# Optimization experiments

Measured on AMD Instinct MI355X. Metric: run time of the kernel, lower is better.

## Reference

```python
import jax, jax.numpy as jnp
import numpy as np

M, N, C, D = 2, 8, 1024, 256  # n_routers, num_adapters, channel_dim, down_sample_size
B, S = 32, 512


def setup_inputs() -> dict:
    key = jax.random.key(0)
    k1, k2, k3, k4, k5 = jax.random.split(key, 5)
    x = jax.random.normal(k1, (B, S, C), dtype=jnp.float32)
    expert_index = jax.random.randint(k2, (M, B), 0, N, dtype=jnp.int32)
    down_w = jax.random.normal(k3, (M, N, C, D), dtype=jnp.float32) * 0.01
    down_b = jax.random.normal(k4, (M, N, D), dtype=jnp.float32) * 0.01
    up_w = jax.random.normal(k5, (M, N, D, C), dtype=jnp.float32) * 0.01
    return {"x": x, "expert_index": expert_index, "down_w": down_w,
            "down_b": down_b, "up_w": up_w}


def reference(x, expert_index, down_w, down_b, up_w):
    # Gather per-(router, batch-element) adapter weights along the adapter axis.
    idx = expert_index  # [M, B]
    bw_down = jnp.take_along_axis(down_w, idx[:, :, None, None], axis=1)  # [M, B, C, D]
    bb_down = jnp.take_along_axis(down_b, idx[:, :, None], axis=1)        # [M, B, D]
    bw_up = jnp.take_along_axis(up_w, idx[:, :, None, None], axis=1)      # [M, B, D, C]
    # z = swish(x @ W_down + b_down)  -> [M, B, S, D]
    z = jnp.einsum('bsc,mbcd->mbsd', x, bw_down) + bb_down[:, :, None, :]
    z = jax.nn.silu(z)
    # u = z @ W_up -> [M, B, S, C]
    u = jnp.einsum('mbsd,mbdc->mbsc', z, bw_up)
    return u
```

## Files before the change

### kernel.cpp

```cpp
#include <hip/hip_runtime.h>
#include <stdint.h>

typedef unsigned short u16;
typedef __bf16 bf16x8 __attribute__((ext_vector_type(8)));
typedef float f32x4 __attribute__((ext_vector_type(4)));

#define MM 2
#define NN 8
#define CC 1024
#define DD 256
#define BB 32
#define SS 512

__device__ __forceinline__ u16 f2bf(float f) {
  uint32_t u = __float_as_uint(f);
  u += 0x7FFFu + ((u >> 16) & 1u);
  return (u16)(u >> 16);
}

__device__ __forceinline__ uint32_t pack2(float a, float b) {
  return (uint32_t)f2bf(a) | ((uint32_t)f2bf(b) << 16);
}

__device__ __forceinline__ void async16(const void* g, void* l) {
  __builtin_amdgcn_global_load_lds(
      (const __attribute__((address_space(1))) uint32_t*)g,
      (__attribute__((address_space(3))) uint32_t*)l, 16, 0, 0);
}

#define T_BLOCKS 4096
__global__ __launch_bounds__(256) void prep_w(
    const float* __restrict__ dw, u16* __restrict__ wdT,
    const float* __restrict__ uw, u16* __restrict__ wuT) {
  const int bid = blockIdx.x;
  __shared__ float tile[32][33];
  const float* src;
  u16* dst;
  int R, L, bx, by, slab;
  if (bid < T_BLOCKS) {
    int t = bid;
    slab = t >> 8;
    int t2 = t & 255;
    bx = t2 & 7;  by = t2 >> 3;
    R = CC; L = DD;
    src = dw; dst = wdT;
  } else {
    int t = bid - T_BLOCKS;
    slab = t >> 8;
    int t2 = t & 255;
    bx = t2 & 31; by = t2 >> 5;
    R = DD; L = CC;
    src = uw; dst = wuT;
  }
  src += (size_t)slab * R * L;
  dst += (size_t)slab * R * L;
  const int c0 = bx * 32, r0 = by * 32;
  const int tx = threadIdx.x & 31, ty = threadIdx.x >> 5;
#pragma unroll
  for (int i = 0; i < 32; i += 8)
    tile[ty + i][tx] = src[(size_t)(r0 + ty + i) * L + c0 + tx];
  __syncthreads();
#pragma unroll
  for (int i = 0; i < 32; i += 8)
    dst[(size_t)(c0 + ty + i) * R + r0 + tx] = f2bf(tile[tx][ty + i]);
}

__global__ __launch_bounds__(512, 2) void fused_adapter(
    const float* __restrict__ x, const u16* __restrict__ wdT,
    const u16* __restrict__ wuT, const float* __restrict__ db,
    const int* __restrict__ eidx, float* __restrict__ out) {
  __shared__ __align__(16) u16 smA[2][128 * 32];
  __shared__ __align__(16) u16 smB[2][256 * 32];
  __shared__ __align__(16) u16 zl[8 * 128 * 32];

  const int pair = blockIdx.y;
  const int m = pair >> 5;
  const int b = pair & 31;
  const int e = eidx[pair];
  const int s0 = blockIdx.x * 128;

  const int tid = threadIdx.x;
  const int lane = tid & 63;
  const int wave = tid >> 6;
  const int quad = lane >> 4;
  const int l16 = lane & 15;

  const int srow = lane >> 2;
  const int kc = (lane & 3) * 8;

  const int wr = (wave >> 2) * 64;
  const int wc = (wave & 3) * 64;

  const u16* Bd = wdT + (size_t)(m * NN + e) * DD * CC;
  const u16* Bu = wuT + (size_t)(m * NN + e) * CC * DD;

  const int arow = tid >> 2;
  const int akseg = (tid & 3) * 8;
  const float* gAx = x + ((size_t)b * SS + s0 + arow) * CC + akseg;
  const int lAoff = arow * 32 + akseg;

  const u16* gB0 = Bd + (size_t)(wave * 32 + srow) * CC + kc;
  const u16* gB1 = Bd + (size_t)(wave * 32 + 16 + srow) * CC + kc;
  const int lB0o = (wave * 32) * 32;
  const int lB1o = (wave * 32 + 16) * 32;

  f32x4 acc[4][4];
#pragma unroll
  for (int i = 0; i < 4; ++i)
#pragma unroll
    for (int j = 0; j < 4; ++j) acc[i][j] = (f32x4){0.f, 0.f, 0.f, 0.f};

  {
    float4 a0 = *reinterpret_cast<const float4*>(gAx + 0);
    float4 a1 = *reinterpret_cast<const float4*>(gAx + 4);
    *reinterpret_cast<uint4*>(&smA[0][lAoff]) =
        make_uint4(pack2(a0.x, a0.y), pack2(a0.z, a0.w),
                   pack2(a1.x, a1.y), pack2(a1.z, a1.w));
  }
  async16(gB0, &smB[0][lB0o]);
  async16(gB1, &smB[0][lB1o]);
  __syncthreads();

  for (int kk = 0; kk < 32; ++kk) {
    const int cur = kk & 1, nxt = cur ^ 1;
    float4 n0, n1;
    if (kk < 31) {
      const int ko = (kk + 1) * 32;
      n0 = *reinterpret_cast<const float4*>(gAx + ko + 0);
      n1 = *reinterpret_cast<const float4*>(gAx + ko + 4);
      async16(gB0 + ko, &smB[nxt][lB0o]);
      async16(gB1 + ko, &smB[nxt][lB1o]);
    } else {
      async16(Bu + (size_t)(wave * 32 + srow) * DD + kc, &smB[nxt][lB0o]);
      async16(Bu + (size_t)(wave * 32 + 16 + srow) * DD + kc, &smB[nxt][lB1o]);
    }
    bf16x8 af[4], bfr[4];
#pragma unroll
    for (int i = 0; i < 4; ++i)
      af[i] = *reinterpret_cast<const bf16x8*>(&smA[cur][(wr + i * 16 + l16) * 32 + quad * 8]);
#pragma unroll
    for (int j = 0; j < 4; ++j)
      bfr[j] = *reinterpret_cast<const bf16x8*>(&smB[cur][(wc + j * 16 + l16) * 32 + quad * 8]);
#pragma unroll
    for (int i = 0; i < 4; ++i)
#pragma unroll
      for (int j = 0; j < 4; ++j)
        acc[i][j] = __builtin_amdgcn_mfma_f32_16x16x32_bf16(af[i], bfr[j], acc[i][j], 0, 0, 0);
    if (kk < 31) {
      *reinterpret_cast<uint4*>(&smA[nxt][lAoff]) =
          make_uint4(pack2(n0.x, n0.y), pack2(n0.z, n0.w),
                     pack2(n1.x, n1.y), pack2(n1.z, n1.w));
    }
    __syncthreads();
  }

  const float* bias_p = db + (size_t)(m * NN + e) * DD;
#pragma unroll
  for (int j = 0; j < 4; ++j) {
    const int d = wc + j * 16 + l16;
    const float bias = bias_p[d];
    const int kt = d >> 5;
    const int kl = d & 31;
#pragma unroll
    for (int i = 0; i < 4; ++i) {
      const int zr = wr + i * 16 + quad * 4;
#pragma unroll
      for (int r = 0; r < 4; ++r) {
        float v = acc[i][j][r] + bias;
        v = v / (1.f + __expf(-v));
        zl[(kt * 128 + zr + r) * 32 + kl] = f2bf(v);
      }
    }
  }
  __syncthreads();

  float* ob = out + ((size_t)pair * SS + s0) * CC;

  for (int g = 0; g < 32; ++g) {
    const int cur2 = g & 1, nxt2 = cur2 ^ 1;
    const int ct = g >> 3;
    const int it = g & 7;
    if (g < 31) {
      const int g2 = g + 1;
      const int ct2 = g2 >> 3;
      const int ko2 = (g2 & 7) * 32;
      async16(Bu + (size_t)(ct2 * 256 + wave * 32 + srow) * DD + ko2 + kc, &smB[nxt2][lB0o]);
      async16(Bu + (size_t)(ct2 * 256 + wave * 32 + 16 + srow) * DD + ko2 + kc, &smB[nxt2][lB1o]);
    }
    if (it == 0) {
#pragma unroll
      for (int i = 0; i < 4; ++i)
#pragma unroll
        for (int j = 0; j < 4; ++j) acc[i][j] = (f32x4){0.f, 0.f, 0.f, 0.f};
    }
    bf16x8 af[4], bfr[4];
#pragma unroll
    for (int i = 0; i < 4; ++i)
      af[i] = *reinterpret_cast<const bf16x8*>(&zl[(it * 128 + wr + i * 16 + l16) * 32 + quad * 8]);
#pragma unroll
    for (int j = 0; j < 4; ++j)
      bfr[j] = *reinterpret_cast<const bf16x8*>(&smB[cur2][(wc + j * 16 + l16) * 32 + quad * 8]);
#pragma unroll
    for (int i = 0; i < 4; ++i)
#pragma unroll
      for (int j = 0; j < 4; ++j)
        acc[i][j] = __builtin_amdgcn_mfma_f32_16x16x32_bf16(af[i], bfr[j], acc[i][j], 0, 0, 0);
    if (it == 7) {
#pragma unroll
      for (int j = 0; j < 4; ++j) {
        const int c = ct * 256 + wc + j * 16 + l16;
#pragma unroll
        for (int i = 0; i < 4; ++i) {
          const int sr = wr + i * 16 + quad * 4;
#pragma unroll
          for (int r = 0; r < 4; ++r)
            ob[(size_t)(sr + r) * CC + c] = acc[i][j][r];
        }
      }
    }
    __syncthreads();
  }
}

extern "C" void kernel_launch(void* const* d_in, const int* in_sizes, int n_in,
                              void* d_out, int out_size, void* d_ws, size_t ws_size,
                              hipStream_t stream) {
  const float* x  = (const float*)d_in[0];
  const int* eidx = (const int*)d_in[1];
  const float* dw = (const float*)d_in[2];
  const float* db = (const float*)d_in[3];
  const float* uw = (const float*)d_in[4];
  float* out = (float*)d_out;

  char* ws = (char*)d_ws;
  u16* wdT = (u16*)(ws);
  u16* wuT = (u16*)(ws + (size_t)8 * 1024 * 1024);

  prep_w<<<dim3(2 * T_BLOCKS), dim3(256), 0, stream>>>(dw, wdT, uw, wuT);
  fused_adapter<<<dim3(SS / 128, MM * BB), dim3(512), 0, stream>>>(
      x, wdT, wuT, db, eidx, out);
}
```

Baseline: 271.5 us.

## Halve row tile, swizzle LDS layouts, interleave routers, widen prep transpose tiles

The fused adapter kernel now processes 64 sequence rows per block instead of 128. This halves the LDS footprint and accumulators so four blocks can share a CU, and it doubles the grid. LDS tiles for x, weights and the intermediate z use an XOR swizzle on the 8-element k-slots to cut bank conflicts, and the block index is remapped so both routers for the same batch element run adjacently and share x in cache. The weight prep kernel transposes 64x32 tiles and writes packed bf16 pairs as 32-bit stores. Smaller tiles mean each block reloads the full per-expert weights for fewer rows, which raises weight traffic.

Result: slower. 278.7 us (+2.7%).

```diff
diff --git a/kernel.cpp b/kernel.cpp
--- a/kernel.cpp
+++ b/kernel.cpp
@@ -28,94 +28,92 @@
       (__attribute__((address_space(3))) uint32_t*)l, 16, 0, 0);
 }
 
-#define T_BLOCKS 4096
 __global__ __launch_bounds__(256) void prep_w(
     const float* __restrict__ dw, u16* __restrict__ wdT,
     const float* __restrict__ uw, u16* __restrict__ wuT) {
-  const int bid = blockIdx.x;
-  __shared__ float tile[32][33];
-  const float* src;
-  u16* dst;
-  int R, L, bx, by, slab;
-  if (bid < T_BLOCKS) {
-    int t = bid;
-    slab = t >> 8;
-    int t2 = t & 255;
-    bx = t2 & 7;  by = t2 >> 3;
-    R = CC; L = DD;
-    src = dw; dst = wdT;
+  __shared__ float tile[64][33];
+  int bid = blockIdx.x;
+  const float* src; u16* dst; int K, N, tk, tn;
+  if (bid < 2048) {
+    K = CC; N = DD;
+    const int slab = bid >> 7, t = bid & 127;
+    tk = t >> 3; tn = t & 7;
+    src = dw + (size_t)slab * K * N;
+    dst = wdT + (size_t)slab * K * N;
   } else {
-    int t = bid - T_BLOCKS;
-    slab = t >> 8;
-    int t2 = t & 255;
-    bx = t2 & 31; by = t2 >> 5;
-    R = DD; L = CC;
-    src = uw; dst = wuT;
-  }
-  src += (size_t)slab * R * L;
-  dst += (size_t)slab * R * L;
-  const int c0 = bx * 32, r0 = by * 32;
+    bid -= 2048;
+    K = DD; N = CC;
+    const int slab = bid >> 7, t = bid & 127;
+    tk = t >> 5; tn = t & 31;
+    src = uw + (size_t)slab * K * N;
+    dst = wuT + (size_t)slab * K * N;
+  }
+  const int k0 = tk * 64, n0 = tn * 32;
   const int tx = threadIdx.x & 31, ty = threadIdx.x >> 5;
 #pragma unroll
-  for (int i = 0; i < 32; i += 8)
-    tile[ty + i][tx] = src[(size_t)(r0 + ty + i) * L + c0 + tx];
+  for (int i = 0; i < 64; i += 8)
+    tile[ty + i][tx] = src[(size_t)(k0 + ty + i) * N + n0 + tx];
   __syncthreads();
-#pragma unroll
-  for (int i = 0; i < 32; i += 8)
-    dst[(size_t)(c0 + ty + i) * R + r0 + tx] = f2bf(tile[tx][ty + i]);
-}
-
-__global__ __launch_bounds__(512, 2) void fused_adapter(
+  uint32_t* dst32 = reinterpret_cast<uint32_t*>(dst);
+#pragma unroll
+  for (int i = 0; i < 32; i += 8) {
+    const int nr = ty + i;
+    dst32[((size_t)(n0 + nr) * K + k0) / 2 + tx] =
+        pack2(tile[2 * tx][nr], tile[2 * tx + 1][nr]);
+  }
+}
+
+__global__ __launch_bounds__(512, 4) void fused_adapter(
     const float* __restrict__ x, const u16* __restrict__ wdT,
     const u16* __restrict__ wuT, const float* __restrict__ db,
     const int* __restrict__ eidx, float* __restrict__ out) {
-  __shared__ __align__(16) u16 smA[2][128 * 32];
+  __shared__ __align__(16) u16 smA[2][64 * 32];
   __shared__ __align__(16) u16 smB[2][256 * 32];
-  __shared__ __align__(16) u16 zl[8 * 128 * 32];
+  __shared__ __align__(16) u16 zl[8 * 64 * 32];
 
   const int pair = blockIdx.y;
-  const int m = pair >> 5;
-  const int b = pair & 31;
-  const int e = eidx[pair];
-  const int s0 = blockIdx.x * 128;
+  const int m = pair & 1;
+  const int b = pair >> 1;
+  const int mb = m * BB + b;
+  const int e = eidx[mb];
+  const int s0 = blockIdx.x * 64;
 
   const int tid = threadIdx.x;
   const int lane = tid & 63;
   const int wave = tid >> 6;
   const int quad = lane >> 4;
   const int l16 = lane & 15;
-
-  const int srow = lane >> 2;
-  const int kc = (lane & 3) * 8;
-
-  const int wr = (wave >> 2) * 64;
+  const int fx = (l16 >> 1) & 3;
+
+  const int wr = (wave >> 2) * 32;
   const int wc = (wave & 3) * 64;
 
   const u16* Bd = wdT + (size_t)(m * NN + e) * DD * CC;
   const u16* Bu = wuT + (size_t)(m * NN + e) * CC * DD;
 
-  const int arow = tid >> 2;
-  const int akseg = (tid & 3) * 8;
+  const int arow = tid >> 3;
+  const int akseg = (tid & 7) * 4;
   const float* gAx = x + ((size_t)b * SS + s0 + arow) * CC + akseg;
-  const int lAoff = arow * 32 + akseg;
-
-  const u16* gB0 = Bd + (size_t)(wave * 32 + srow) * CC + kc;
-  const u16* gB1 = Bd + (size_t)(wave * 32 + 16 + srow) * CC + kc;
-  const int lB0o = (wave * 32) * 32;
-  const int lB1o = (wave * 32 + 16) * 32;
-
-  f32x4 acc[4][4];
-#pragma unroll
-  for (int i = 0; i < 4; ++i)
+  const int lAoff = arow * 32 +
+                    ((((tid & 7) >> 1) ^ ((arow >> 1) & 3)) * 8) + (tid & 1) * 4;
+
+  const int srow = lane >> 2;
+  const int qx = (lane & 3) ^ ((srow >> 1) & 3);
+  const u16* gB0 = Bd + (size_t)(wave * 32 + srow) * CC + qx * 8;
+  const u16* gB1 = gB0 + (size_t)16 * CC;
+  const int lB0o = wave * 32 * 32;
+  const int lB1o = lB0o + 16 * 32;
+
+  f32x4 acc[2][4];
+#pragma unroll
+  for (int i = 0; i < 2; ++i)
 #pragma unroll
     for (int j = 0; j < 4; ++j) acc[i][j] = (f32x4){0.f, 0.f, 0.f, 0.f};
 
   {
-    float4 a0 = *reinterpret_cast<const float4*>(gAx + 0);
-    float4 a1 = *reinterpret_cast<const float4*>(gAx + 4);
-    *reinterpret_cast<uint4*>(&smA[0][lAoff]) =
-        make_uint4(pack2(a0.x, a0.y), pack2(a0.z, a0.w),
-                   pack2(a1.x, a1.y), pack2(a1.z, a1.w));
+    float4 a0 = *reinterpret_cast<const float4*>(gAx);
+    uint2 w; w.x = pack2(a0.x, a0.y); w.y = pack2(a0.z, a0.w);
+    *reinterpret_cast<uint2*>(&smA[0][lAoff]) = w;
   }
   async16(gB0, &smB[0][lB0o]);
   async16(gB1, &smB[0][lB1o]);
@@ -123,33 +121,33 @@
 
   for (int kk = 0; kk < 32; ++kk) {
     const int cur = kk & 1, nxt = cur ^ 1;
-    float4 n0, n1;
+    float4 nA;
     if (kk < 31) {
       const int ko = (kk + 1) * 32;
-      n0 = *reinterpret_cast<const float4*>(gAx + ko + 0);
-      n1 = *reinterpret_cast<const float4*>(gAx + ko + 4);
+      nA = *reinterpret_cast<const float4*>(gAx + ko);
       async16(gB0 + ko, &smB[nxt][lB0o]);
       async16(gB1 + ko, &smB[nxt][lB1o]);
     } else {
-      async16(Bu + (size_t)(wave * 32 + srow) * DD + kc, &smB[nxt][lB0o]);
-      async16(Bu + (size_t)(wave * 32 + 16 + srow) * DD + kc, &smB[nxt][lB1o]);
-    }
-    bf16x8 af[4], bfr[4];
-#pragma unroll
-    for (int i = 0; i < 4; ++i)
-      af[i] = *reinterpret_cast<const bf16x8*>(&smA[cur][(wr + i * 16 + l16) * 32 + quad * 8]);
+      async16(Bu + (size_t)(wave * 32 + srow) * DD + qx * 8, &smB[nxt][lB0o]);
+      async16(Bu + (size_t)(wave * 32 + 16 + srow) * DD + qx * 8, &smB[nxt][lB1o]);
+    }
+    bf16x8 af[2], bfr[4];
+#pragma unroll
+    for (int i = 0; i < 2; ++i)
+      af[i] = *reinterpret_cast<const bf16x8*>(
+          &smA[cur][(wr + i * 16 + l16) * 32 + (quad ^ fx) * 8]);
 #pragma unroll
     for (int j = 0; j < 4; ++j)
-      bfr[j] = *reinterpret_cast<const bf16x8*>(&smB[cur][(wc + j * 16 + l16) * 32 + quad * 8]);
-#pragma unroll
-    for (int i = 0; i < 4; ++i)
+      bfr[j] = *reinterpret_cast<const bf16x8*>(
+          &smB[cur][(wc + j * 16 + l16) * 32 + (quad ^ fx) * 8]);
+#pragma unroll
+    for (int i = 0; i < 2; ++i)
 #pragma unroll
       for (int j = 0; j < 4; ++j)
         acc[i][j] = __builtin_amdgcn_mfma_f32_16x16x32_bf16(af[i], bfr[j], acc[i][j], 0, 0, 0);
     if (kk < 31) {
-      *reinterpret_cast<uint4*>(&smA[nxt][lAoff]) =
-          make_uint4(pack2(n0.x, n0.y), pack2(n0.z, n0.w),
-                     pack2(n1.x, n1.y), pack2(n1.z, n1.w));
+      uint2 w; w.x = pack2(nA.x, nA.y); w.y = pack2(nA.z, nA.w);
+      *reinterpret_cast<uint2*>(&smA[nxt][lAoff]) = w;
     }
     __syncthreads();
   }
@@ -161,20 +159,23 @@
     const float bias = bias_p[d];
     const int kt = d >> 5;
     const int kl = d & 31;
-#pragma unroll
-    for (int i = 0; i < 4; ++i) {
+    const int slot0 = kl >> 3;
+    const int kin = kl & 7;
+#pragma unroll
+    for (int i = 0; i < 2; ++i) {
       const int zr = wr + i * 16 + quad * 4;
 #pragma unroll
       for (int r = 0; r < 4; ++r) {
+        const int row = zr + r;
         float v = acc[i][j][r] + bias;
         v = v / (1.f + __expf(-v));
-        zl[(kt * 128 + zr + r) * 32 + kl] = f2bf(v);
+        zl[kt * 2048 + row * 32 + ((slot0 ^ ((row >> 1) & 3)) * 8) + kin] = f2bf(v);
       }
     }
   }
   __syncthreads();
 
-  float* ob = out + ((size_t)pair * SS + s0) * CC;
+  float* ob = out + ((size_t)mb * SS + s0) * CC;
 
   for (int g = 0; g < 32; ++g) {
     const int cur2 = g & 1, nxt2 = cur2 ^ 1;
@@ -183,25 +184,29 @@
     if (g < 31) {
       const int g2 = g + 1;
       const int ct2 = g2 >> 3;
-      const int ko2 = (g2 & 7) * 32;
-      async16(Bu + (size_t)(ct2 * 256 + wave * 32 + srow) * DD + ko2 + kc, &smB[nxt2][lB0o]);
-      async16(Bu + (size_t)(ct2 * 256 + wave * 32 + 16 + srow) * DD + ko2 + kc, &smB[nxt2][lB1o]);
+      const int io2 = (g2 & 7) * 32;
+      async16(Bu + (size_t)(ct2 * 256 + wave * 32 + srow) * DD + io2 + qx * 8,
+              &smB[nxt2][lB0o]);
+      async16(Bu + (size_t)(ct2 * 256 + wave * 32 + 16 + srow) * DD + io2 + qx * 8,
+              &smB[nxt2][lB1o]);
     }
     if (it == 0) {
 #pragma unroll
-      for (int i = 0; i < 4; ++i)
+      for (int i = 0; i < 2; ++i)
 #pragma unroll
         for (int j = 0; j < 4; ++j) acc[i][j] = (f32x4){0.f, 0.f, 0.f, 0.f};
     }
-    bf16x8 af[4], bfr[4];
-#pragma unroll
-    for (int i = 0; i < 4; ++i)
-      af[i] = *reinterpret_cast<const bf16x8*>(&zl[(it * 128 + wr + i * 16 + l16) * 32 + quad * 8]);
+    bf16x8 af[2], bfr[4];
+#pragma unroll
+    for (int i = 0; i < 2; ++i)
+      af[i] = *reinterpret_cast<const bf16x8*>(
+          &zl[it * 2048 + (wr + i * 16 + l16) * 32 + (quad ^ fx) * 8]);
 #pragma unroll
     for (int j = 0; j < 4; ++j)
-      bfr[j] = *reinterpret_cast<const bf16x8*>(&smB[cur2][(wc + j * 16 + l16) * 32 + quad * 8]);
-#pragma unroll
-    for (int i = 0; i < 4; ++i)
+      bfr[j] = *reinterpret_cast<const bf16x8*>(
+          &smB[cur2][(wc + j * 16 + l16) * 32 + (quad ^ fx) * 8]);
+#pragma unroll
+    for (int i = 0; i < 2; ++i)
 #pragma unroll
       for (int j = 0; j < 4; ++j)
         acc[i][j] = __builtin_amdgcn_mfma_f32_16x16x32_bf16(af[i], bfr[j], acc[i][j], 0, 0, 0);
@@ -210,7 +215,7 @@
       for (int j = 0; j < 4; ++j) {
         const int c = ct * 256 + wc + j * 16 + l16;
 #pragma unroll
-        for (int i = 0; i < 4; ++i) {
+        for (int i = 0; i < 2; ++i) {
           const int sr = wr + i * 16 + quad * 4;
 #pragma unroll
           for (int r = 0; r < 4; ++r)
@@ -236,7 +241,7 @@
   u16* wdT = (u16*)(ws);
   u16* wuT = (u16*)(ws + (size_t)8 * 1024 * 1024);
 
-  prep_w<<<dim3(2 * T_BLOCKS), dim3(256), 0, stream>>>(dw, wdT, uw, wuT);
-  fused_adapter<<<dim3(SS / 128, MM * BB), dim3(512), 0, stream>>>(
+  prep_w<<<dim3(4096), dim3(256), 0, stream>>>(dw, wdT, uw, wuT);
+  fused_adapter<<<dim3(SS / 64, MM * BB), dim3(512), 0, stream>>>(
       x, wdT, wuT, db, eidx, out);
 }
```
